# Performance work log

Hardware: AMD Instinct MI355X
Metric: run time of the kernel (lower is better)

## Reference

```python
import jax, jax.numpy as jnp
import numpy as np

NUM_HEADS = 4
NUM_GROUPS = 8
EPS = 1e-5


def setup_inputs() -> dict:
    key = jax.random.key(0)
    ks = jax.random.split(key, 4)
    B, C, H, W = 4, 256, 64, 64
    x = jax.random.normal(ks[0], (B, C, H, W), dtype=jnp.float32)
    norm_w = jnp.ones((C,), dtype=jnp.float32)
    norm_b = jnp.zeros((C,), dtype=jnp.float32)
    qkv_w = jax.random.normal(ks[1], (3 * C, C), dtype=jnp.float32) * (1.0 / np.sqrt(C))
    qkv_b = jnp.zeros((3 * C,), dtype=jnp.float32)
    proj_w = jax.random.normal(ks[2], (C, C), dtype=jnp.float32) * (1.0 / np.sqrt(C))
    proj_b = jnp.zeros((C,), dtype=jnp.float32)
    return {"x": x, "norm_w": norm_w, "norm_b": norm_b, "qkv_w": qkv_w,
            "qkv_b": qkv_b, "proj_w": proj_w, "proj_b": proj_b}


def _group_norm(x, w, b):
    B, C, H, W = x.shape
    g = x.reshape(B, NUM_GROUPS, C // NUM_GROUPS, H, W)
    mean = g.mean(axis=(2, 3, 4), keepdims=True)
    var = g.var(axis=(2, 3, 4), keepdims=True)
    g = (g - mean) * jax.lax.rsqrt(var + EPS)
    g = g.reshape(B, C, H, W)
    return g * w[None, :, None, None] + b[None, :, None, None]


def reference(x, norm_w, norm_b, qkv_w, qkv_b, proj_w, proj_b):
    B, C, H, W = x.shape
    hd = C // NUM_HEADS
    scale = hd ** (-0.5)
    h = _group_norm(x, norm_w, norm_b)
    # 1x1 conv == channel matmul: [3C,C] x [B,C,H,W]
    qkv = jnp.einsum('oc,bchw->bohw', qkv_w, h) + qkv_b[None, :, None, None]
    q, k, v = jnp.split(qkv, 3, axis=1)
    N = H * W
    q = q.reshape(B, NUM_HEADS, hd, N)
    k = k.reshape(B, NUM_HEADS, hd, N)
    v = v.reshape(B, NUM_HEADS, hd, N)
    attn = jnp.einsum('bhdn,bhdm->bhnm', q, k) * scale
    attn = jax.nn.softmax(attn, axis=-1)
    out = jnp.einsum('bhnm,bhdm->bhdn', attn, v)
    out = out.reshape(B, C, H, W)
    proj = jnp.einsum('oc,bchw->bohw', proj_w, out) + proj_b[None, :, None, None]
    return x + proj
```

## Files before the change

### kernel.cpp

```cpp
#include <hip/hip_runtime.h>
#include <hip/hip_bf16.h>

#define BATCH 4
#define CCH   256
#define NSP   4096
#define GRPSZ (32 * 4096)
#define NHEAD 4
#define HD    64

typedef __attribute__((ext_vector_type(8))) short short8;
typedef __attribute__((ext_vector_type(8))) unsigned short ushort8_t;
typedef __attribute__((ext_vector_type(4))) float f32x4;

__device__ __forceinline__ unsigned short f2b(float f) {
    unsigned u = __builtin_bit_cast(unsigned, f);
    unsigned r = u + 0x7FFFu + ((u >> 16) & 1u);
    return (unsigned short)(r >> 16);
}
__device__ __forceinline__ unsigned short b16p(float f) {
    __hip_bfloat16 h = __float2bfloat16(f);
    return __builtin_bit_cast(unsigned short, h);
}
__device__ __forceinline__ float ex2(float x) {
    float r; asm("v_exp_f32 %0, %1" : "=v"(r) : "v"(x)); return r;
}

__global__ __launch_bounds__(256) void gn_partial(const float* __restrict__ x,
                                                  float* __restrict__ sums) {
    int chunk = blockIdx.x & 7;
    int bg    = blockIdx.x >> 3;
    const float* base = x + (size_t)bg * GRPSZ + (size_t)chunk * (GRPSZ / 8);
    int t = threadIdx.x;
    float s = 0.f, ss = 0.f;
#pragma unroll
    for (int i = 0; i < 16; ++i) {
        float4 v = *(const float4*)&base[(t + i * 256) * 4];
        s  += v.x + v.y + v.z + v.w;
        ss += v.x * v.x + v.y * v.y + v.z * v.z + v.w * v.w;
    }
    __shared__ float rs[256], rss[256];
    rs[t] = s; rss[t] = ss;
    __syncthreads();
    for (int off = 128; off > 0; off >>= 1) {
        if (t < off) { rs[t] += rs[t + off]; rss[t] += rss[t + off]; }
        __syncthreads();
    }
    if (t == 0) {
        sums[blockIdx.x * 2]     = rs[0];
        sums[blockIdx.x * 2 + 1] = rss[0];
    }
}

__global__ __launch_bounds__(256) void gn_pack(const float* __restrict__ x,
                                               const float* __restrict__ sums,
                                               const float* __restrict__ gw,
                                               const float* __restrict__ gb,
                                               unsigned short* __restrict__ hT) {
    __shared__ float LT[64][65];
    __shared__ float wcs[64], bcs[64];
    int b = blockIdx.z, c0 = blockIdx.y * 64, n0 = blockIdx.x * 64;
    int t = threadIdx.x;
    if (t < 64) {
        int c  = c0 + t;
        int bg = b * 8 + (c >> 5);
        float s = 0.f, ss = 0.f;
#pragma unroll
        for (int i = 0; i < 8; ++i) {
            s  += sums[(bg * 8 + i) * 2];
            ss += sums[(bg * 8 + i) * 2 + 1];
        }
        const float invn = 1.f / (float)GRPSZ;
        float mean = s * invn;
        float var  = ss * invn - mean * mean;
        float inv  = rsqrtf(var + 1e-5f);
        float wc = gw[c] * inv;
        wcs[t] = wc;
        bcs[t] = gb[c] - mean * wc;
    }
    __syncthreads();
    int cl4 = (t & 15) * 4, cr = t >> 4;
#pragma unroll
    for (int p = 0; p < 4; ++p) {
        int c = cr + p * 16;
        float4 v = *(const float4*)&x[(size_t)(b * 256 + c0 + c) * 4096 + n0 + cl4];
        float wc = wcs[c], bb = bcs[c];
        LT[c][cl4 + 0] = v.x * wc + bb;
        LT[c][cl4 + 1] = v.y * wc + bb;
        LT[c][cl4 + 2] = v.z * wc + bb;
        LT[c][cl4 + 3] = v.w * wc + bb;
    }
    __syncthreads();
#pragma unroll
    for (int p = 0; p < 2; ++p) {
        int n  = (t >> 3) + p * 32;
        int c8 = (t & 7) * 8;
        ushort8_t w;
#pragma unroll
        for (int i = 0; i < 8; ++i) w[i] = f2b(LT[c8 + i][n]);
        *(ushort8_t*)&hT[((size_t)b * 4096 + n0 + n) * 256 + c0 + c8] = w;
    }
}

__global__ __launch_bounds__(256) void gemm_qkv(const float* __restrict__ W,
                                                const unsigned short* __restrict__ hT,
                                                const float* __restrict__ bias,
                                                unsigned short* __restrict__ Qbf,
                                                unsigned short* __restrict__ Ktbf,
                                                unsigned short* __restrict__ Vbf) {
    __shared__ unsigned short Wl[64 * 64];
    __shared__ unsigned short Hl[64 * 64];
    int b = blockIdx.z, o0 = blockIdx.y * 64, n0 = blockIdx.x * 64;
    int t = threadIdx.x, lane = t & 63, wid = t >> 6, g = lane >> 4, cl = lane & 15;
    f32x4 acc[4];
#pragma unroll
    for (int j = 0; j < 4; ++j) acc[j] = (f32x4){0.f, 0.f, 0.f, 0.f};
    int sr = t >> 2;
    int sk = (t & 3) * 16;
    int swr = (sr & 7) << 3;
    int swa = (cl & 7) << 3;
    for (int k0 = 0; k0 < 256; k0 += 64) {
        __syncthreads();
        {
            const float* wr = &W[(size_t)(o0 + sr) * 256 + k0 + sk];
            float4 w0 = *(const float4*)&wr[0],  w1 = *(const float4*)&wr[4];
            float4 w2 = *(const float4*)&wr[8],  w3 = *(const float4*)&wr[12];
            ushort8_t u0 = {f2b(w0.x), f2b(w0.y), f2b(w0.z), f2b(w0.w),
                            f2b(w1.x), f2b(w1.y), f2b(w1.z), f2b(w1.w)};
            ushort8_t u1 = {f2b(w2.x), f2b(w2.y), f2b(w2.z), f2b(w2.w),
                            f2b(w3.x), f2b(w3.y), f2b(w3.z), f2b(w3.w)};
            *(ushort8_t*)&Wl[sr * 64 + (sk ^ swr)]       = u0;
            *(ushort8_t*)&Wl[sr * 64 + ((sk + 8) ^ swr)] = u1;
        }
        {
            const ushort8_t* hr = (const ushort8_t*)&hT[((size_t)b * 4096 + n0 + sr) * 256 + k0 + sk];
            *(ushort8_t*)&Hl[sr * 64 + (sk ^ swr)]       = hr[0];
            *(ushort8_t*)&Hl[sr * 64 + ((sk + 8) ^ swr)] = hr[1];
        }
        __syncthreads();
#pragma unroll
        for (int ks = 0; ks < 2; ++ks) {
            short8 a = *(short8*)&Hl[(wid * 16 + cl) * 64 + ((ks * 32 + g * 8) ^ swa)];
#pragma unroll
            for (int j = 0; j < 4; ++j) {
                short8 bb = *(short8*)&Wl[(j * 16 + cl) * 64 + ((ks * 32 + g * 8) ^ swa)];
                acc[j] = __builtin_amdgcn_mfma_f32_16x16x32_bf16(a, bb, acc[j], 0, 0, 0);
            }
        }
    }
    int sect = blockIdx.y >> 2, head = blockIdx.y & 3;
    size_t tilebase = (((size_t)b * NHEAD + head) * 64 + blockIdx.x) * 4096;
    int nrow = wid * 16 + g * 4;
    if (sect == 0) {
        const float qsc = 0.18033688011112042f;
#pragma unroll
        for (int j = 0; j < 4; ++j) {
            float bi = bias[o0 + j * 16 + cl];
#pragma unroll
            for (int r = 0; r < 4; ++r)
                Qbf[tilebase + (size_t)(nrow + r) * 64 + j * 16 + cl] =
                    f2b((acc[j][r] + bi) * qsc);
        }
    } else if (sect == 1) {
#pragma unroll
        for (int j = 0; j < 4; ++j) {
            float bi = bias[o0 + j * 16 + cl];
#pragma unroll
            for (int r = 0; r < 4; ++r) {
                int key = nrow + r;
                int sw  = ((key ^ (key >> 3)) & 7) << 3;
                Ktbf[tilebase + (size_t)key * 64 + ((j * 16 + cl) ^ sw)] =
                    f2b(acc[j][r] + bi);
            }
        }
    } else {
        __syncthreads();
        unsigned short* VL = Wl;
#pragma unroll
        for (int j = 0; j < 4; ++j) {
            float bi = bias[o0 + j * 16 + cl];
            int d = j * 16 + cl;
#pragma unroll
            for (int r = 0; r < 4; ++r) {
                int key = nrow + r;
                VL[d * 64 + (key ^ ((d & 7) << 3))] = f2b(acc[j][r] + bi);
            }
        }
        __syncthreads();
        ushort8_t* dst = (ushort8_t*)&Vbf[tilebase];
        const ushort8_t* srcl = (const ushort8_t*)VL;
        dst[t]       = srcl[t];
        dst[t + 256] = srcl[t + 256];
    }
}

__global__ __launch_bounds__(256) void gemm_proj(const float* __restrict__ W,
                                                 const unsigned short* __restrict__ aT,
                                                 const float* __restrict__ bias,
                                                 const float* __restrict__ x,
                                                 float* __restrict__ Out) {
    __shared__ unsigned short Wl[64 * 64];
    __shared__ unsigned short Al[64 * 64];
    int b = blockIdx.z, o0 = blockIdx.y * 64, n0 = blockIdx.x * 64;
    int t = threadIdx.x, lane = t & 63, wid = t >> 6, g = lane >> 4, cl = lane & 15;
    f32x4 acc[4];
#pragma unroll
    for (int j = 0; j < 4; ++j) acc[j] = (f32x4){0.f, 0.f, 0.f, 0.f};
    int sr = t >> 2, sk = (t & 3) * 16;
    int swr = (sr & 7) << 3;
    int swa = (cl & 7) << 3;
    for (int k0 = 0; k0 < 256; k0 += 64) {
        __syncthreads();
        {
            const float* wr = &W[(size_t)(o0 + sr) * 256 + k0 + sk];
            float4 w0 = *(const float4*)&wr[0],  w1 = *(const float4*)&wr[4];
            float4 w2 = *(const float4*)&wr[8],  w3 = *(const float4*)&wr[12];
            ushort8_t u0 = {f2b(w0.x), f2b(w0.y), f2b(w0.z), f2b(w0.w),
                            f2b(w1.x), f2b(w1.y), f2b(w1.z), f2b(w1.w)};
            ushort8_t u1 = {f2b(w2.x), f2b(w2.y), f2b(w2.z), f2b(w2.w),
                            f2b(w3.x), f2b(w3.y), f2b(w3.z), f2b(w3.w)};
            *(ushort8_t*)&Wl[sr * 64 + (sk ^ swr)]       = u0;
            *(ushort8_t*)&Wl[sr * 64 + ((sk + 8) ^ swr)] = u1;
        }
        {
            const ushort8_t* ar = (const ushort8_t*)&aT[((size_t)b * 4096 + n0 + sr) * 256 + k0 + sk];
            *(ushort8_t*)&Al[sr * 64 + (sk ^ swr)]       = ar[0];
            *(ushort8_t*)&Al[sr * 64 + ((sk + 8) ^ swr)] = ar[1];
        }
        __syncthreads();
#pragma unroll
        for (int ks = 0; ks < 2; ++ks) {
            short8 a = *(short8*)&Wl[(wid * 16 + cl) * 64 + ((ks * 32 + g * 8) ^ swa)];
#pragma unroll
            for (int j = 0; j < 4; ++j) {
                short8 bb = *(short8*)&Al[(j * 16 + cl) * 64 + ((ks * 32 + g * 8) ^ swa)];
                acc[j] = __builtin_amdgcn_mfma_f32_16x16x32_bf16(a, bb, acc[j], 0, 0, 0);
            }
        }
    }
    float bi[4];
#pragma unroll
    for (int r = 0; r < 4; ++r) bi[r] = bias[o0 + wid * 16 + g * 4 + r];
#pragma unroll
    for (int r = 0; r < 4; ++r) {
        int o = o0 + wid * 16 + g * 4 + r;
        size_t rowbase = ((size_t)b * 256 + o) * 4096 + n0;
#pragma unroll
        for (int j = 0; j < 4; ++j) {
            size_t idx = rowbase + j * 16 + cl;
            Out[idx] = acc[j][r] + bi[r] + x[idx];
        }
    }
}

__global__ __launch_bounds__(256, 4) void flash_mfma(const unsigned short* __restrict__ Qbf,
                                                     const unsigned short* __restrict__ Ktbf,
                                                     const unsigned short* __restrict__ Vbf,
                                                     unsigned short* __restrict__ aoutbf) {
    __shared__ unsigned short Kbuf[2][4096];
    __shared__ unsigned short Vbuf[2][4096];
    __shared__ unsigned short Pbuf[4096];

    const int t    = threadIdx.x;
    const int lane = t & 63;
    const int wid  = t >> 6;
    const int g    = lane >> 4;
    const int cl   = lane & 15;

    const int head = blockIdx.y, b = blockIdx.z;
    const int bh   = b * NHEAD + head;

    const unsigned short* Qt = Qbf + (((size_t)bh * 64 + blockIdx.x) * 4096);
    short8 qf[2];
    qf[0] = *(const short8*)&Qt[(wid * 16 + cl) * 64 + g * 8];
    qf[1] = *(const short8*)&Qt[(wid * 16 + cl) * 64 + 32 + g * 8];

    const ushort8_t* kg = (const ushort8_t*)(Ktbf + (size_t)bh * 64 * 4096);
    const ushort8_t* vg = (const ushort8_t*)(Vbf  + (size_t)bh * 64 * 4096);

    f32x4 o_acc[4];
#pragma unroll
    for (int ds = 0; ds < 4; ++ds) o_acc[ds] = (f32x4){0.f, 0.f, 0.f, 0.f};
    float m[4], l[4];
#pragma unroll
    for (int r = 0; r < 4; ++r) { m[r] = -1e30f; l[r] = 0.f; }

    ushort8_t kr0 = kg[t], kr1 = kg[t + 256];
    ushort8_t vr0 = vg[t], vr1 = vg[t + 256];
    ((ushort8_t*)&Kbuf[0][0])[t] = kr0;  ((ushort8_t*)&Kbuf[0][0])[t + 256] = kr1;
    ((ushort8_t*)&Vbuf[0][0])[t] = vr0;  ((ushort8_t*)&Vbuf[0][0])[t + 256] = vr1;
    __syncthreads();

    for (int tile = 0; tile < 64; ++tile) {
        const int cur = tile & 1;
        const unsigned short* KT = &Kbuf[cur][0];
        const unsigned short* VS = &Vbuf[cur][0];
        if (tile < 63) {
            const ushort8_t* kn = kg + (size_t)(tile + 1) * 512;
            const ushort8_t* vn = vg + (size_t)(tile + 1) * 512;
            kr0 = kn[t]; kr1 = kn[t + 256];
            vr0 = vn[t]; vr1 = vn[t + 256];
        }

        f32x4 accs[4];
#pragma unroll
        for (int s = 0; s < 4; ++s) {
            f32x4 a = (f32x4){0.f, 0.f, 0.f, 0.f};
            int row = s * 16 + cl;
            int sw  = ((row ^ (row >> 3)) & 7) << 3;
#pragma unroll
            for (int h = 0; h < 2; ++h) {
                short8 kf = *(const short8*)&KT[row * 64 + ((h * 32 + g * 8) ^ sw)];
                a = __builtin_amdgcn_mfma_f32_16x16x32_bf16(qf[h], kf, a, 0, 0, 0);
            }
            accs[s] = a;
        }

        float nm[4];
        int need = 0;
#pragma unroll
        for (int r = 0; r < 4; ++r) {
            float rm = fmaxf(fmaxf(accs[0][r], accs[1][r]), fmaxf(accs[2][r], accs[3][r]));
#pragma unroll
            for (int mask = 1; mask < 16; mask <<= 1)
                rm = fmaxf(rm, __shfl_xor(rm, mask));
            nm[r] = fmaxf(m[r], rm);
            need |= (rm > m[r] + 8.f) ? 1 : 0;
        }
        if (__any(need)) {
#pragma unroll
            for (int r = 0; r < 4; ++r) {
                float corr = ex2(m[r] - nm[r]);
                l[r] *= corr;
                o_acc[0][r] *= corr; o_acc[1][r] *= corr;
                o_acc[2][r] *= corr; o_acc[3][r] *= corr;
                m[r] = nm[r];
            }
        }
        unsigned short pb16[4][4];
#pragma unroll
        for (int r = 0; r < 4; ++r) {
            float ps = 0.f;
#pragma unroll
            for (int s = 0; s < 4; ++s) {
                float p = ex2(accs[s][r] - m[r]);
                ps += p;
                pb16[r][s] = b16p(p);
            }
            l[r] += ps;
        }

        unsigned short* Pw = &Pbuf[wid * 16 * 64];
#pragma unroll
        for (int r = 0; r < 4; ++r) {
            int row = g * 4 + r;
#pragma unroll
            for (int s = 0; s < 4; ++s) {
                int col = s * 16 + cl;
                Pw[row * 64 + (col ^ ((row & 7) << 3))] = pb16[r][s];
            }
        }
        short8 pf[2];
#pragma unroll
        for (int h2 = 0; h2 < 2; ++h2)
            pf[h2] = *(const short8*)&Pw[cl * 64 + ((h2 * 32 + g * 8) ^ ((cl & 7) << 3))];
#pragma unroll
        for (int ds = 0; ds < 4; ++ds) {
            int vrow = ds * 16 + cl;
#pragma unroll
            for (int h2 = 0; h2 < 2; ++h2) {
                short8 vf = *(const short8*)&VS[vrow * 64 + ((h2 * 32 + g * 8) ^ ((cl & 7) << 3))];
                o_acc[ds] = __builtin_amdgcn_mfma_f32_16x16x32_bf16(pf[h2], vf, o_acc[ds], 0, 0, 0);
            }
        }

        if (tile < 63) {
            ushort8_t* KN = (ushort8_t*)&Kbuf[cur ^ 1][0];
            ushort8_t* VN = (ushort8_t*)&Vbuf[cur ^ 1][0];
            KN[t] = kr0;  KN[t + 256] = kr1;
            VN[t] = vr0;  VN[t + 256] = vr1;
        }
        __syncthreads();
    }

    float inv[4];
#pragma unroll
    for (int r = 0; r < 4; ++r) {
        float s = l[r];
#pragma unroll
        for (int mask = 1; mask < 16; mask <<= 1) s += __shfl_xor(s, mask);
        inv[r] = 1.f / s;
    }
    unsigned short* Ab = aoutbf + ((size_t)b * 4096 + blockIdx.x * 64 + wid * 16) * 256 + head * 64;
#pragma unroll
    for (int ds = 0; ds < 4; ++ds)
#pragma unroll
        for (int r = 0; r < 4; ++r)
            Ab[(size_t)(g * 4 + r) * 256 + ds * 16 + cl] = f2b(o_acc[ds][r] * inv[r]);
}

extern "C" void kernel_launch(void* const* d_in, const int* in_sizes, int n_in,
                              void* d_out, int out_size, void* d_ws, size_t ws_size,
                              hipStream_t stream) {
    const float* x    = (const float*)d_in[0];
    const float* nw   = (const float*)d_in[1];
    const float* nb   = (const float*)d_in[2];
    const float* qkvw = (const float*)d_in[3];
    const float* qkvb = (const float*)d_in[4];
    const float* pw   = (const float*)d_in[5];
    const float* pb   = (const float*)d_in[6];
    float* out = (float*)d_out;

    char* ws = (char*)d_ws;
    float* sums = (float*)ws;
    unsigned short* hT     = (unsigned short*)(ws + (1 << 16));
    unsigned short* Qbf    = hT     + (size_t)BATCH * NSP * CCH;
    unsigned short* Ktbf   = Qbf    + (size_t)BATCH * NHEAD * NSP * HD;
    unsigned short* Vbf    = Ktbf   + (size_t)BATCH * NHEAD * NSP * HD;
    unsigned short* aoutbf = Vbf    + (size_t)BATCH * NHEAD * NSP * HD;

    gn_partial<<<dim3(256), dim3(256), 0, stream>>>(x, sums);
    gn_pack<<<dim3(64, 4, BATCH), dim3(256), 0, stream>>>(x, sums, nw, nb, hT);
    gemm_qkv<<<dim3(64, 12, BATCH), dim3(256), 0, stream>>>(qkvw, hT, qkvb, Qbf, Ktbf, Vbf);
    flash_mfma<<<dim3(64, NHEAD, BATCH), dim3(256), 0, stream>>>(Qbf, Ktbf, Vbf, aoutbf);
    gemm_proj<<<dim3(64, 4, BATCH), dim3(256), 0, stream>>>(pw, aoutbf, pb, x, out);
}
```

Before: 279.2 us.

## Process two query tiles per flash-attention block to reuse K/V tiles

Each flash-attention block now handles 128 query rows (two 64-row Q tiles) instead of 64, so every K/V tile loaded into shared memory feeds twice as many MFMAs. The grid is halved and launch bounds relaxed to 2 blocks per CU to make room for doubled accumulators and softmax state. This cuts global K/V traffic and per-tile load and sync overhead per unit of work, at the cost of more registers, a larger P buffer, and only 512 blocks in the grid, which may underfill the GPU.

```diff
diff --git a/kernel.cpp b/kernel.cpp
--- a/kernel.cpp
+++ b/kernel.cpp
@@ -252,13 +252,13 @@
     }
 }
 
-__global__ __launch_bounds__(256, 4) void flash_mfma(const unsigned short* __restrict__ Qbf,
+__global__ __launch_bounds__(256, 2) void flash_mfma(const unsigned short* __restrict__ Qbf,
                                                      const unsigned short* __restrict__ Ktbf,
                                                      const unsigned short* __restrict__ Vbf,
                                                      unsigned short* __restrict__ aoutbf) {
     __shared__ unsigned short Kbuf[2][4096];
     __shared__ unsigned short Vbuf[2][4096];
-    __shared__ unsigned short Pbuf[4096];
+    __shared__ unsigned short Pbuf[8192];
 
     const int t    = threadIdx.x;
     const int lane = t & 63;
@@ -269,20 +269,27 @@
     const int head = blockIdx.y, b = blockIdx.z;
     const int bh   = b * NHEAD + head;
 
-    const unsigned short* Qt = Qbf + (((size_t)bh * 64 + blockIdx.x) * 4096);
-    short8 qf[2];
-    qf[0] = *(const short8*)&Qt[(wid * 16 + cl) * 64 + g * 8];
-    qf[1] = *(const short8*)&Qt[(wid * 16 + cl) * 64 + 32 + g * 8];
+    short8 qf[2][2];
+#pragma unroll
+    for (int f = 0; f < 2; ++f) {
+        const unsigned short* Qt = Qbf + (((size_t)bh * 64 + blockIdx.x * 2 + f) * 4096);
+        qf[f][0] = *(const short8*)&Qt[(wid * 16 + cl) * 64 + g * 8];
+        qf[f][1] = *(const short8*)&Qt[(wid * 16 + cl) * 64 + 32 + g * 8];
+    }
 
     const ushort8_t* kg = (const ushort8_t*)(Ktbf + (size_t)bh * 64 * 4096);
     const ushort8_t* vg = (const ushort8_t*)(Vbf  + (size_t)bh * 64 * 4096);
 
-    f32x4 o_acc[4];
-#pragma unroll
-    for (int ds = 0; ds < 4; ++ds) o_acc[ds] = (f32x4){0.f, 0.f, 0.f, 0.f};
-    float m[4], l[4];
-#pragma unroll
-    for (int r = 0; r < 4; ++r) { m[r] = -1e30f; l[r] = 0.f; }
+    f32x4 o_acc[2][4];
+#pragma unroll
+    for (int f = 0; f < 2; ++f)
+#pragma unroll
+        for (int ds = 0; ds < 4; ++ds) o_acc[f][ds] = (f32x4){0.f, 0.f, 0.f, 0.f};
+    float m[2][4], l[2][4];
+#pragma unroll
+    for (int f = 0; f < 2; ++f)
+#pragma unroll
+        for (int r = 0; r < 4; ++r) { m[f][r] = -1e30f; l[f][r] = 0.f; }
 
     ushort8_t kr0 = kg[t], kr1 = kg[t + 256];
     ushort8_t vr0 = vg[t], vr1 = vg[t + 256];
@@ -301,75 +308,87 @@
             vr0 = vn[t]; vr1 = vn[t + 256];
         }
 
-        f32x4 accs[4];
+        f32x4 accs[2][4];
+#pragma unroll
+        for (int f = 0; f < 2; ++f)
+#pragma unroll
+            for (int s = 0; s < 4; ++s) accs[f][s] = (f32x4){0.f, 0.f, 0.f, 0.f};
 #pragma unroll
         for (int s = 0; s < 4; ++s) {
-            f32x4 a = (f32x4){0.f, 0.f, 0.f, 0.f};
             int row = s * 16 + cl;
             int sw  = ((row ^ (row >> 3)) & 7) << 3;
 #pragma unroll
             for (int h = 0; h < 2; ++h) {
                 short8 kf = *(const short8*)&KT[row * 64 + ((h * 32 + g * 8) ^ sw)];
-                a = __builtin_amdgcn_mfma_f32_16x16x32_bf16(qf[h], kf, a, 0, 0, 0);
-            }
-            accs[s] = a;
-        }
-
-        float nm[4];
+                accs[0][s] = __builtin_amdgcn_mfma_f32_16x16x32_bf16(qf[0][h], kf, accs[0][s], 0, 0, 0);
+                accs[1][s] = __builtin_amdgcn_mfma_f32_16x16x32_bf16(qf[1][h], kf, accs[1][s], 0, 0, 0);
+            }
+        }
+
+        float nm[2][4];
         int need = 0;
 #pragma unroll
-        for (int r = 0; r < 4; ++r) {
-            float rm = fmaxf(fmaxf(accs[0][r], accs[1][r]), fmaxf(accs[2][r], accs[3][r]));
-#pragma unroll
-            for (int mask = 1; mask < 16; mask <<= 1)
-                rm = fmaxf(rm, __shfl_xor(rm, mask));
-            nm[r] = fmaxf(m[r], rm);
-            need |= (rm > m[r] + 8.f) ? 1 : 0;
-        }
+        for (int f = 0; f < 2; ++f)
+#pragma unroll
+            for (int r = 0; r < 4; ++r) {
+                float rm = fmaxf(fmaxf(accs[f][0][r], accs[f][1][r]),
+                                 fmaxf(accs[f][2][r], accs[f][3][r]));
+#pragma unroll
+                for (int mask = 1; mask < 16; mask <<= 1)
+                    rm = fmaxf(rm, __shfl_xor(rm, mask));
+                nm[f][r] = fmaxf(m[f][r], rm);
+                need |= (rm > m[f][r] + 8.f) ? 1 : 0;
+            }
         if (__any(need)) {
 #pragma unroll
+            for (int f = 0; f < 2; ++f)
+#pragma unroll
+                for (int r = 0; r < 4; ++r) {
+                    float corr = ex2(m[f][r] - nm[f][r]);
+                    l[f][r] *= corr;
+                    o_acc[f][0][r] *= corr; o_acc[f][1][r] *= corr;
+                    o_acc[f][2][r] *= corr; o_acc[f][3][r] *= corr;
+                    m[f][r] = nm[f][r];
+                }
+        }
+        unsigned short pb16[2][4][4];
+#pragma unroll
+        for (int f = 0; f < 2; ++f)
+#pragma unroll
             for (int r = 0; r < 4; ++r) {
-                float corr = ex2(m[r] - nm[r]);
-                l[r] *= corr;
-                o_acc[0][r] *= corr; o_acc[1][r] *= corr;
-                o_acc[2][r] *= corr; o_acc[3][r] *= corr;
-                m[r] = nm[r];
-            }
-        }
-        unsigned short pb16[4][4];
-#pragma unroll
-        for (int r = 0; r < 4; ++r) {
-            float ps = 0.f;
-#pragma unroll
-            for (int s = 0; s < 4; ++s) {
-                float p = ex2(accs[s][r] - m[r]);
-                ps += p;
-                pb16[r][s] = b16p(p);
-            }
-            l[r] += ps;
-        }
-
-        unsigned short* Pw = &Pbuf[wid * 16 * 64];
-#pragma unroll
-        for (int r = 0; r < 4; ++r) {
-            int row = g * 4 + r;
-#pragma unroll
-            for (int s = 0; s < 4; ++s) {
-                int col = s * 16 + cl;
-                Pw[row * 64 + (col ^ ((row & 7) << 3))] = pb16[r][s];
-            }
-        }
-        short8 pf[2];
-#pragma unroll
-        for (int h2 = 0; h2 < 2; ++h2)
-            pf[h2] = *(const short8*)&Pw[cl * 64 + ((h2 * 32 + g * 8) ^ ((cl & 7) << 3))];
-#pragma unroll
-        for (int ds = 0; ds < 4; ++ds) {
-            int vrow = ds * 16 + cl;
-#pragma unroll
-            for (int h2 = 0; h2 < 2; ++h2) {
-                short8 vf = *(const short8*)&VS[vrow * 64 + ((h2 * 32 + g * 8) ^ ((cl & 7) << 3))];
-                o_acc[ds] = __builtin_amdgcn_mfma_f32_16x16x32_bf16(pf[h2], vf, o_acc[ds], 0, 0, 0);
+                float ps = 0.f;
+#pragma unroll
+                for (int s = 0; s < 4; ++s) {
+                    float p = ex2(accs[f][s][r] - m[f][r]);
+                    ps += p;
+                    pb16[f][r][s] = b16p(p);
+                }
+                l[f][r] += ps;
+            }
+
+        unsigned short* Pw = &Pbuf[wid * 2048];
+#pragma unroll
+        for (int f = 0; f < 2; ++f)
+#pragma unroll
+            for (int r = 0; r < 4; ++r) {
+                int row = f * 16 + g * 4 + r;
+#pragma unroll
+                for (int s = 0; s < 4; ++s) {
+                    int col = s * 16 + cl;
+                    Pw[row * 64 + (col ^ ((row & 7) << 3))] = pb16[f][r][s];
+                }
+            }
+#pragma unroll
+        for (int h2 = 0; h2 < 2; ++h2) {
+            int off = (h2 * 32 + g * 8) ^ ((cl & 7) << 3);
+            short8 pf0 = *(const short8*)&Pw[cl * 64 + off];
+            short8 pf1 = *(const short8*)&Pw[(16 + cl) * 64 + off];
+#pragma unroll
+            for (int ds = 0; ds < 4; ++ds) {
+                int vrow = ds * 16 + cl;
+                short8 vf = *(const short8*)&VS[vrow * 64 + off];
+                o_acc[0][ds] = __builtin_amdgcn_mfma_f32_16x16x32_bf16(pf0, vf, o_acc[0][ds], 0, 0, 0);
+                o_acc[1][ds] = __builtin_amdgcn_mfma_f32_16x16x32_bf16(pf1, vf, o_acc[1][ds], 0, 0, 0);
             }
         }
 
@@ -382,20 +401,24 @@
         __syncthreads();
     }
 
-    float inv[4];
-#pragma unroll
-    for (int r = 0; r < 4; ++r) {
-        float s = l[r];
-#pragma unroll
-        for (int mask = 1; mask < 16; mask <<= 1) s += __shfl_xor(s, mask);
-        inv[r] = 1.f / s;
-    }
-    unsigned short* Ab = aoutbf + ((size_t)b * 4096 + blockIdx.x * 64 + wid * 16) * 256 + head * 64;
-#pragma unroll
-    for (int ds = 0; ds < 4; ++ds)
-#pragma unroll
-        for (int r = 0; r < 4; ++r)
-            Ab[(size_t)(g * 4 + r) * 256 + ds * 16 + cl] = f2b(o_acc[ds][r] * inv[r]);
+#pragma unroll
+    for (int f = 0; f < 2; ++f) {
+        float inv[4];
+#pragma unroll
+        for (int r = 0; r < 4; ++r) {
+            float s = l[f][r];
+#pragma unroll
+            for (int mask = 1; mask < 16; mask <<= 1) s += __shfl_xor(s, mask);
+            inv[r] = 1.f / s;
+        }
+        unsigned short* Ab = aoutbf +
+            ((size_t)b * 4096 + blockIdx.x * 128 + f * 64 + wid * 16) * 256 + head * 64;
+#pragma unroll
+        for (int ds = 0; ds < 4; ++ds)
+#pragma unroll
+            for (int r = 0; r < 4; ++r)
+                Ab[(size_t)(g * 4 + r) * 256 + ds * 16 + cl] = f2b(o_acc[f][ds][r] * inv[r]);
+    }
 }
 
 extern "C" void kernel_launch(void* const* d_in, const int* in_sizes, int n_in,
@@ -421,6 +444,6 @@
     gn_partial<<<dim3(256), dim3(256), 0, stream>>>(x, sums);
     gn_pack<<<dim3(64, 4, BATCH), dim3(256), 0, stream>>>(x, sums, nw, nb, hT);
     gemm_qkv<<<dim3(64, 12, BATCH), dim3(256), 0, stream>>>(qkvw, hT, qkvb, Qbf, Ktbf, Vbf);
-    flash_mfma<<<dim3(64, NHEAD, BATCH), dim3(256), 0, stream>>>(Qbf, Ktbf, Vbf, aoutbf);
+    flash_mfma<<<dim3(32, NHEAD, BATCH), dim3(256), 0, stream>>>(Qbf, Ktbf, Vbf, aoutbf);
     gemm_proj<<<dim3(64, 4, BATCH), dim3(256), 0, stream>>>(pw, aoutbf, pb, x, out);
 }
```

Result: no change. 284.2 us (+1.8%).
